# Kernel optimization log

Hardware: AMD Instinct MI355X
Metric: run time of the kernel (lower is better)

Reference implementation:

```python
import jax, jax.numpy as jnp
import numpy as np

HIDDEN = 1024
H = 16        # query heads
HK = 4        # kv heads
G = H // HK   # GQA group size
D = 64        # head dim
EPS = 1e-6


def rmsnorm(x, w):
    # normalize over last dim (head_dim)
    var = jnp.mean(jnp.square(x), axis=-1, keepdims=True)
    return x * jax.lax.rsqrt(var + EPS) * w


def setup_inputs() -> dict:
    key = jax.random.key(0)
    ks = jax.random.split(key, 8)
    B, S_KV, S_Q = 2, 4096, 512
    inputs = jax.random.normal(ks[0], (B, S_KV, HIDDEN), dtype=jnp.float32)
    latent = jax.random.normal(ks[1], (B, S_Q, HIDDEN), dtype=jnp.float32)
    # xavier_uniform-style init: limit = sqrt(6/(fan_in+fan_out))
    def xavier(k, shape, gain=1.0):
        fan_out, fan_in = shape
        limit = gain * np.sqrt(6.0 / (fan_in + fan_out))
        return jax.random.uniform(k, shape, jnp.float32, -limit, limit)
    wq = xavier(ks[2], (H * D, HIDDEN))
    wk = xavier(ks[3], (HK * D, HIDDEN))
    wv = xavier(ks[4], (HK * D, HIDDEN))
    wo = xavier(ks[5], (HIDDEN, H * D), gain=1.0 / np.sqrt(2.0))
    q_norm_w = jnp.ones((D,), jnp.float32)
    k_norm_w = jnp.ones((D,), jnp.float32)
    return {"inputs": inputs, "latent": latent, "wq": wq, "wk": wk,
            "wv": wv, "wo": wo, "q_norm_w": q_norm_w, "k_norm_w": k_norm_w}


def reference(inputs, latent, wq, wk, wv, wo, q_norm_w, k_norm_w):
    B, S_q, _ = latent.shape
    S_kv = inputs.shape[1]
    # projections (Linear: x @ W^T)
    q = (latent @ wq.T).reshape(B, S_q, H, D)    # [B,Sq,H,D]
    k = (inputs @ wk.T).reshape(B, S_kv, HK, D)  # [B,Skv,Hk,D]
    v = (inputs @ wv.T).reshape(B, S_kv, HK, D)
    q = rmsnorm(q, q_norm_w)
    k = rmsnorm(k, k_norm_w)
    # GQA without materializing repeated K/V: view q as [B,Hk,G,Sq,D]
    q = q.transpose(0, 2, 1, 3).reshape(B, HK, G, S_q, D)
    k = k.transpose(0, 2, 1, 3)  # [B,Hk,Skv,D]
    v = v.transpose(0, 2, 1, 3)  # [B,Hk,Skv,D]
    # NOTE: no 1/sqrt(D) scaling, faithful to the source module
    scores = jnp.einsum('bkgqd,bksd->bkgqs', q, k)  # [B,Hk,G,Sq,Skv]
    attn = jax.nn.softmax(scores.astype(jnp.float32), axis=-1).astype(q.dtype)
    out = jnp.einsum('bkgqs,bksd->bkgqd', attn, v)  # [B,Hk,G,Sq,D]
    # back to [B,Sq,H*D]
    out = out.reshape(B, H, S_q, D).transpose(0, 2, 1, 3).reshape(B, S_q, H * D)
    return out @ wo.T
```

## Files before the change

kernel.cpp:

```cpp
#include <hip/hip_runtime.h>

#define NB 2
#define SQ 512
#define SKV 4096
#define HID 1024
#define NH 16
#define NHK 4
#define NG 4
#define HD 64
#define EPSF 1e-6f
#define NSPLIT 4
#define RB (NB * NH * SQ)

typedef short v8s __attribute__((ext_vector_type(8)));
typedef short v4s __attribute__((ext_vector_type(4)));
typedef float v4f __attribute__((ext_vector_type(4)));
typedef float v2f __attribute__((ext_vector_type(2)));

static __device__ __forceinline__ short f2bf(float f) {
  unsigned u = __builtin_bit_cast(unsigned, f);
  u += 0x7FFFu + ((u >> 16) & 1u);
  return (short)(u >> 16);
}

static __device__ __forceinline__ v8s lds_frag(const short* lds, int row, int kbyte) {
  return *(const v8s*)((const char*)lds + row * 128 + (kbyte ^ ((row & 7) << 4)));
}

template<int SRC_F32, int NIT>
static __device__ __forceinline__ void stage_tile(const void* src, int ld,
                                                  int r0, int c0, short* lds, int t) {
#pragma unroll
  for (int i = 0; i < NIT; ++i) {
    int flat = t * 8 + i * 2048;
    int row = flat >> 6, col = flat & 63;
    v8s v;
    if (SRC_F32) {
      const float* p = (const float*)src + (size_t)(r0 + row) * ld + c0 + col;
      v4f a = *(const v4f*)p;
      v4f b = *(const v4f*)(p + 4);
      v[0] = f2bf(a[0]); v[1] = f2bf(a[1]); v[2] = f2bf(a[2]); v[3] = f2bf(a[3]);
      v[4] = f2bf(b[0]); v[5] = f2bf(b[1]); v[6] = f2bf(b[2]); v[7] = f2bf(b[3]);
    } else {
      v = *(const v8s*)((const short*)src + (size_t)(r0 + row) * ld + c0 + col);
    }
    *(v8s*)((char*)lds + row * 128 + ((col * 2) ^ ((row & 7) << 4))) = v;
  }
}

__global__ __launch_bounds__(256) void proj_all(const float* __restrict__ inputs,
                                                const float* __restrict__ latent,
                                                const float* __restrict__ wq,
                                                const float* __restrict__ wk,
                                                const float* __restrict__ wv,
                                                const float* __restrict__ qnw,
                                                const float* __restrict__ knw,
                                                short* __restrict__ Qb,
                                                short* __restrict__ Kb,
                                                short* __restrict__ Vtb) {
  __shared__ __align__(16) short Asm[128 * 64];
  __shared__ __align__(16) short Bsm[128 * 64];
  const int bid = blockIdx.x;
  const int t = threadIdx.x, lane = t & 63, w = t >> 6;
  const int l15 = lane & 15, g4 = lane >> 4;
  v4f acc[2][4] = {};

  if (bid < 512) {
    const int xcd = bid & 7, slot = bid >> 3;
    const int mblk = xcd * 8 + (slot >> 3);
    const int zh = slot & 7;
    const int z = zh & 1, head = zh >> 1;
    const int m0 = mblk * 128;
    const float* W = z ? wv : wk;
    for (int k0 = 0; k0 < HID; k0 += 64) {
      __syncthreads();
      stage_tile<1, 4>(inputs, HID, m0, k0, Asm, t);
      stage_tile<1, 2>(W, HID, head * 64, k0, Bsm, t);
      __syncthreads();
      v8s af[2][2], bfr[4][2];
#pragma unroll
      for (int mf = 0; mf < 2; ++mf)
#pragma unroll
        for (int s = 0; s < 2; ++s)
          af[mf][s] = lds_frag(Asm, w * 32 + mf * 16 + l15, s * 64 + g4 * 16);
#pragma unroll
      for (int nf = 0; nf < 4; ++nf)
#pragma unroll
        for (int s = 0; s < 2; ++s)
          bfr[nf][s] = lds_frag(Bsm, nf * 16 + l15, s * 64 + g4 * 16);
#pragma unroll
      for (int mf = 0; mf < 2; ++mf)
#pragma unroll
        for (int nf = 0; nf < 4; ++nf)
#pragma unroll
          for (int s = 0; s < 2; ++s)
            acc[mf][nf] = __builtin_amdgcn_mfma_f32_16x16x32_bf16(af[mf][s], bfr[nf][s],
                                                                  acc[mf][nf], 0, 0, 0);
    }
    if (!z) {
      float wcol[4];
#pragma unroll
      for (int nf = 0; nf < 4; ++nf) wcol[nf] = knw[nf * 16 + l15];
#pragma unroll
      for (int mf = 0; mf < 2; ++mf)
#pragma unroll
        for (int j = 0; j < 4; ++j) {
          float ss = acc[mf][0][j] * acc[mf][0][j] + acc[mf][1][j] * acc[mf][1][j] +
                     acc[mf][2][j] * acc[mf][2][j] + acc[mf][3][j] * acc[mf][3][j];
#pragma unroll
          for (int msk = 1; msk < 16; msk <<= 1) ss += __shfl_xor(ss, msk);
          float sc = rsqrtf(ss * (1.0f / 64.0f) + EPSF);
          int m = m0 + w * 32 + mf * 16 + g4 * 4 + j;
          int b = m >> 12, sl = m & (SKV - 1);
          size_t base = ((size_t)(b * NHK + head) * SKV + sl) * 64;
#pragma unroll
          for (int nf = 0; nf < 4; ++nf)
            Kb[base + nf * 16 + l15] = f2bf(acc[mf][nf][j] * sc * wcol[nf]);
        }
    } else {
#pragma unroll
      for (int mf = 0; mf < 2; ++mf) {
        int m = m0 + w * 32 + mf * 16 + g4 * 4;
        int b = m >> 12, sl = m & (SKV - 1);
#pragma unroll
        for (int nf = 0; nf < 4; ++nf) {
          int d = nf * 16 + l15;
          v4s o;
#pragma unroll
          for (int j = 0; j < 4; ++j) o[j] = f2bf(acc[mf][nf][j]);
          *(v4s*)(Vtb + ((size_t)(b * NHK + head) * 64 + d) * SKV + sl) = o;
        }
      }
    }
  } else {
    const int r = bid - 512;
    const int xcd = r & 7, slot = r >> 3;
    const int nblk = (slot & 1) | ((xcd & 3) << 1);
    const int mblk = ((slot >> 1) & 7) | ((xcd >> 2) << 3);
    const int m0 = mblk * 64;
    const int wr = w >> 1, wc = w & 1;
    for (int k0 = 0; k0 < HID; k0 += 64) {
      __syncthreads();
      stage_tile<1, 2>(latent, HID, m0, k0, Asm, t);
      stage_tile<1, 4>(wq, HID, nblk * 128, k0, Bsm, t);
      __syncthreads();
      v8s af[2][2], bfr[4][2];
#pragma unroll
      for (int mf = 0; mf < 2; ++mf)
#pragma unroll
        for (int s = 0; s < 2; ++s)
          af[mf][s] = lds_frag(Asm, wr * 32 + mf * 16 + l15, s * 64 + g4 * 16);
#pragma unroll
      for (int nf = 0; nf < 4; ++nf)
#pragma unroll
        for (int s = 0; s < 2; ++s)
          bfr[nf][s] = lds_frag(Bsm, wc * 64 + nf * 16 + l15, s * 64 + g4 * 16);
#pragma unroll
      for (int mf = 0; mf < 2; ++mf)
#pragma unroll
        for (int nf = 0; nf < 4; ++nf)
#pragma unroll
          for (int s = 0; s < 2; ++s)
            acc[mf][nf] = __builtin_amdgcn_mfma_f32_16x16x32_bf16(af[mf][s], bfr[nf][s],
                                                                  acc[mf][nf], 0, 0, 0);
    }
    const int head = nblk * 2 + wc;
    float wcol[4];
#pragma unroll
    for (int nf = 0; nf < 4; ++nf) wcol[nf] = qnw[nf * 16 + l15];
#pragma unroll
    for (int mf = 0; mf < 2; ++mf)
#pragma unroll
      for (int j = 0; j < 4; ++j) {
        float ss = acc[mf][0][j] * acc[mf][0][j] + acc[mf][1][j] * acc[mf][1][j] +
                   acc[mf][2][j] * acc[mf][2][j] + acc[mf][3][j] * acc[mf][3][j];
#pragma unroll
        for (int msk = 1; msk < 16; msk <<= 1) ss += __shfl_xor(ss, msk);
        float sc = rsqrtf(ss * (1.0f / 64.0f) + EPSF);
        int m = m0 + wr * 32 + mf * 16 + g4 * 4 + j;
        int b = m >> 9, sl = m & (SQ - 1);
        size_t base = ((size_t)(b * NH + head) * SQ + sl) * 64;
#pragma unroll
        for (int nf = 0; nf < 4; ++nf)
          Qb[base + nf * 16 + l15] = f2bf(acc[mf][nf][j] * sc * wcol[nf]);
      }
  }
}

__global__ __launch_bounds__(256) void wo_gemm(const short* __restrict__ Ab,
                                               const float* __restrict__ Wo,
                                               float* __restrict__ Wop) {
  __shared__ __align__(16) short Asm[64 * 64];
  __shared__ __align__(16) short Bsm[128 * 64];
  const int t = threadIdx.x, lane = t & 63, w = t >> 6;
  const int l15 = lane & 15, g4 = lane >> 4;
  const int wr = w >> 1, wc = w & 1;
  const int p = blockIdx.x;
  const int nblk = p & 7, slot = p >> 3;
  const int m0 = (slot & 15) * 64, n0 = nblk * 128, ks = slot >> 4;
  v4f acc[2][4] = {};
  for (int kk = 0; kk < 4; ++kk) {
    int k0 = ks * 256 + kk * 64;
    __syncthreads();
    stage_tile<0, 2>(Ab, HID, m0, k0, Asm, t);
    stage_tile<1, 4>(Wo, HID, n0, k0, Bsm, t);
    __syncthreads();
    v8s af[2][2], bfr[4][2];
#pragma unroll
    for (int mf = 0; mf < 2; ++mf)
#pragma unroll
      for (int s = 0; s < 2; ++s)
        af[mf][s] = lds_frag(Asm, wr * 32 + mf * 16 + l15, s * 64 + g4 * 16);
#pragma unroll
    for (int nf = 0; nf < 4; ++nf)
#pragma unroll
      for (int s = 0; s < 2; ++s)
        bfr[nf][s] = lds_frag(Bsm, wc * 64 + nf * 16 + l15, s * 64 + g4 * 16);
#pragma unroll
    for (int mf = 0; mf < 2; ++mf)
#pragma unroll
      for (int nf = 0; nf < 4; ++nf)
#pragma unroll
        for (int s = 0; s < 2; ++s)
          acc[mf][nf] = __builtin_amdgcn_mfma_f32_16x16x32_bf16(af[mf][s], bfr[nf][s],
                                                                acc[mf][nf], 0, 0, 0);
  }
  float* C = Wop + (size_t)ks * HID * NB * SQ;
#pragma unroll
  for (int mf = 0; mf < 2; ++mf)
#pragma unroll
    for (int j = 0; j < 4; ++j) {
      int m = m0 + wr * 32 + mf * 16 + g4 * 4 + j;
#pragma unroll
      for (int nf = 0; nf < 4; ++nf)
        C[(size_t)m * HID + n0 + wc * 64 + nf * 16 + l15] = acc[mf][nf][j];
    }
}

__global__ __launch_bounds__(256) void wo_reduce(const float* __restrict__ Wop,
                                                 float* __restrict__ out) {
  int idx = (blockIdx.x * 256 + threadIdx.x) * 4;
  v4f s = *(const v4f*)(Wop + idx);
#pragma unroll
  for (int ks = 1; ks < 4; ++ks) {
    v4f p = *(const v4f*)(Wop + (size_t)ks * HID * NB * SQ + idx);
    s[0] += p[0]; s[1] += p[1]; s[2] += p[2]; s[3] += p[3];
  }
  *(v4f*)(out + idx) = s;
}

__global__ __launch_bounds__(256) void attn_kernel(const short* __restrict__ Qb,
                                                   const short* __restrict__ Kb,
                                                   const short* __restrict__ Vt,
                                                   float* __restrict__ Op,
                                                   float* __restrict__ Ml) {
  __shared__ __align__(16) short Ksm[2][64 * 64];
  __shared__ __align__(16) short Vsm[2][64 * 64];
  __shared__ __align__(16) short Psm[4][16 * 64];
  int id = blockIdx.x;
  int qt = id & 31, hk = (id >> 5) & 3, b = (id >> 7) & 1, sp = id >> 8;
  int t = threadIdx.x, w = t >> 6, lane = t & 63;
  int l15 = lane & 15, g4 = lane >> 4;
  int h = hk * NG + w;

  const short* qbase = Qb + (((size_t)(b * NH + h)) * SQ + qt * 16) * 64;
  v8s aq[2];
#pragma unroll
  for (int s = 0; s < 2; ++s)
    aq[s] = *(const v8s*)(qbase + (size_t)l15 * 64 + s * 32 + g4 * 8);

  const short* kbase = Kb + ((size_t)(b * NHK + hk)) * SKV * 64;
  const short* vbase = Vt + ((size_t)(b * NHK + hk)) * 64 * SKV;
  char* pbase = (char*)&Psm[w][0];

  v4f acco[4] = {};
  float mrow[4], lrow[4];
#pragma unroll
  for (int r = 0; r < 4; ++r) { mrow[r] = -__builtin_inff(); lrow[r] = 0.f; }

  const int KV0 = sp * (SKV / NSPLIT);
  for (int kt = 0; kt < SKV / NSPLIT / 128; ++kt) {
    int kv0 = KV0 + kt * 128;
    __syncthreads();
    stage_tile<0, 2>(kbase, 64, kv0, 0, Ksm[0], t);
    stage_tile<0, 2>(kbase, 64, kv0 + 64, 0, Ksm[1], t);
    stage_tile<0, 2>(vbase, SKV, 0, kv0, Vsm[0], t);
    stage_tile<0, 2>(vbase, SKV, 0, kv0 + 64, Vsm[1], t);
    __syncthreads();

    v4f accs[8] = {};
#pragma unroll
    for (int hf = 0; hf < 2; ++hf)
#pragma unroll
      for (int f = 0; f < 4; ++f)
#pragma unroll
        for (int s = 0; s < 2; ++s) {
          v8s bk = lds_frag(Ksm[hf], f * 16 + l15, s * 64 + g4 * 16);
          accs[hf * 4 + f] =
              __builtin_amdgcn_mfma_f32_16x16x32_bf16(aq[s], bk, accs[hf * 4 + f], 0, 0, 0);
        }

    float tm[4];
#pragma unroll
    for (int r = 0; r < 4; ++r) {
      float m01 = fmaxf(accs[0][r], accs[1][r]), m23 = fmaxf(accs[2][r], accs[3][r]);
      float m45 = fmaxf(accs[4][r], accs[5][r]), m67 = fmaxf(accs[6][r], accs[7][r]);
      tm[r] = fmaxf(fmaxf(m01, m23), fmaxf(m45, m67));
    }
#pragma unroll
    for (int msk = 1; msk < 16; msk <<= 1)
#pragma unroll
      for (int r = 0; r < 4; ++r)
        tm[r] = fmaxf(tm[r], __shfl_xor(tm[r], msk));
    float al[4];
#pragma unroll
    for (int r = 0; r < 4; ++r) {
      float mn = fmaxf(mrow[r], tm[r]);
      al[r] = __expf(mrow[r] - mn);
      mrow[r] = mn;
    }
    float rs[4] = {0.f, 0.f, 0.f, 0.f};
#pragma unroll
    for (int f = 0; f < 8; ++f)
#pragma unroll
      for (int r = 0; r < 4; ++r) {
        accs[f][r] = __expf(accs[f][r] - mrow[r]);
        rs[r] += accs[f][r];
      }
#pragma unroll
    for (int msk = 1; msk < 16; msk <<= 1)
#pragma unroll
      for (int r = 0; r < 4; ++r) rs[r] += __shfl_xor(rs[r], msk);
#pragma unroll
    for (int r = 0; r < 4; ++r) lrow[r] = lrow[r] * al[r] + rs[r];
#pragma unroll
    for (int fd = 0; fd < 4; ++fd)
#pragma unroll
      for (int r = 0; r < 4; ++r) acco[fd][r] *= al[r];

#pragma unroll
    for (int hf = 0; hf < 2; ++hf) {
#pragma unroll
      for (int f = 0; f < 4; ++f)
#pragma unroll
        for (int r = 0; r < 4; ++r) {
          int row = g4 * 4 + r;
          int colB = (f * 16 + l15) * 2;
          *(short*)(pbase + row * 128 + (colB ^ ((row & 7) << 4))) = f2bf(accs[hf * 4 + f][r]);
        }
      asm volatile("s_waitcnt lgkmcnt(0)" ::: "memory");
      __builtin_amdgcn_sched_barrier(0);
      v8s pa[2];
#pragma unroll
      for (int s = 0; s < 2; ++s)
        pa[s] = *(const v8s*)(pbase + l15 * 128 + ((s * 64 + g4 * 16) ^ ((l15 & 7) << 4)));
      asm volatile("s_waitcnt lgkmcnt(0)" ::: "memory");
      __builtin_amdgcn_sched_barrier(0);
#pragma unroll
      for (int fd = 0; fd < 4; ++fd)
#pragma unroll
        for (int s = 0; s < 2; ++s) {
          v8s vb = lds_frag(Vsm[hf], fd * 16 + l15, s * 64 + g4 * 16);
          acco[fd] = __builtin_amdgcn_mfma_f32_16x16x32_bf16(pa[s], vb, acco[fd], 0, 0, 0);
        }
    }
  }

  size_t rowbase = ((size_t)b * NH + h) * SQ + qt * 16;
#pragma unroll
  for (int fd = 0; fd < 4; ++fd)
#pragma unroll
    for (int r = 0; r < 4; ++r) {
      int row = g4 * 4 + r;
      Op[((size_t)sp * RB + rowbase + row) * 64 + fd * 16 + l15] = acco[fd][r];
    }
  if (l15 == 0) {
#pragma unroll
    for (int r = 0; r < 4; ++r) {
      int row = g4 * 4 + r;
      v2f ml; ml[0] = mrow[r]; ml[1] = lrow[r];
      *(v2f*)(Ml + ((size_t)sp * RB + rowbase + row) * 2) = ml;
    }
  }
}

__global__ __launch_bounds__(256) void merge_attn(const float* __restrict__ Op,
                                                  const float* __restrict__ Ml,
                                                  short* __restrict__ Ab) {
  int idx = blockIdx.x * 256 + threadIdx.x;
  int d = idx & 63, row = idx >> 6;
  float ms[NSPLIT], ls[NSPLIT];
  float M = -__builtin_inff();
#pragma unroll
  for (int s = 0; s < NSPLIT; ++s) {
    v2f ml = *(const v2f*)(Ml + ((size_t)s * RB + row) * 2);
    ms[s] = ml[0]; ls[s] = ml[1];
    M = fmaxf(M, ms[s]);
  }
  float L = 0.f, o = 0.f;
#pragma unroll
  for (int s = 0; s < NSPLIT; ++s) {
    float wgt = __expf(ms[s] - M);
    L += ls[s] * wgt;
    o += wgt * Op[((size_t)s * RB + row) * 64 + d];
  }
  int b = row >> 13;
  int hh = (row >> 9) & 15;
  int sq = row & 511;
  Ab[((size_t)(b * SQ + sq)) * HID + hh * 64 + d] = f2bf(o / L);
}

extern "C" void kernel_launch(void* const* d_in, const int* in_sizes, int n_in,
                              void* d_out, int out_size, void* d_ws, size_t ws_size,
                              hipStream_t stream) {
  const float* inputs = (const float*)d_in[0];
  const float* latent = (const float*)d_in[1];
  const float* wq = (const float*)d_in[2];
  const float* wk = (const float*)d_in[3];
  const float* wv = (const float*)d_in[4];
  const float* wo = (const float*)d_in[5];
  const float* qnw = (const float*)d_in[6];
  const float* knw = (const float*)d_in[7];

  char* ws = (char*)d_ws;
  float* Op  = (float*)(ws);
  float* Wop = (float*)(ws);
  float* Ml  = (float*)(ws + 16777216);
  short* Qb  = (short*)(ws + 17825792);
  short* Kb  = (short*)(ws + 19922944);
  short* Vtb = (short*)(ws + 24117248);
  short* Ab  = (short*)(ws + 28311552);

  proj_all<<<640, 256, 0, stream>>>(inputs, latent, wq, wk, wv, qnw, knw, Qb, Kb, Vtb);
  attn_kernel<<<256 * NSPLIT, 256, 0, stream>>>(Qb, Kb, Vtb, Op, Ml);
  merge_attn<<<RB * 64 / 256, 256, 0, stream>>>(Op, Ml, Ab);
  wo_gemm<<<512, 256, 0, stream>>>(Ab, wo, Wop);
  wo_reduce<<<1024, 256, 0, stream>>>(Wop, (float*)d_out);
}
```

Before: 213.9 us.

## Double-buffer LDS with register prefetch in projection and output GEMMs

Adds software pipelining to the projection and Wo GEMM kernels. Global loads for the next K tile are issued into registers before the current tile's MFMAs run, and are converted and written into the other LDS buffer afterwards. This drops one barrier per iteration and hides global-load latency behind compute. In exchange, LDS use rises to two 24KB buffers and register pressure grows from the prefetch registers, which may lower occupancy. The attention kernel only gets a renamed staging helper.

```diff
diff --git a/kernel.cpp b/kernel.cpp
--- a/kernel.cpp
+++ b/kernel.cpp
@@ -27,26 +27,68 @@
   return *(const v8s*)((const char*)lds + row * 128 + (kbyte ^ ((row & 7) << 4)));
 }
 
-template<int SRC_F32, int NIT>
-static __device__ __forceinline__ void stage_tile(const void* src, int ld,
-                                                  int r0, int c0, short* lds, int t) {
+template<int NIT>
+static __device__ __forceinline__ void stage_load_f32(const float* src, int ld,
+                                                      int r0, int c0, int t, v4f* regs) {
 #pragma unroll
   for (int i = 0; i < NIT; ++i) {
     int flat = t * 8 + i * 2048;
     int row = flat >> 6, col = flat & 63;
+    const float* p = src + (size_t)(r0 + row) * ld + c0 + col;
+    regs[2 * i] = *(const v4f*)p;
+    regs[2 * i + 1] = *(const v4f*)(p + 4);
+  }
+}
+
+template<int NIT>
+static __device__ __forceinline__ void stage_write_bf16(const v4f* regs, short* lds, int t) {
+#pragma unroll
+  for (int i = 0; i < NIT; ++i) {
+    int flat = t * 8 + i * 2048;
+    int row = flat >> 6, col = flat & 63;
+    v4f a = regs[2 * i], b = regs[2 * i + 1];
     v8s v;
-    if (SRC_F32) {
-      const float* p = (const float*)src + (size_t)(r0 + row) * ld + c0 + col;
-      v4f a = *(const v4f*)p;
-      v4f b = *(const v4f*)(p + 4);
-      v[0] = f2bf(a[0]); v[1] = f2bf(a[1]); v[2] = f2bf(a[2]); v[3] = f2bf(a[3]);
-      v[4] = f2bf(b[0]); v[5] = f2bf(b[1]); v[6] = f2bf(b[2]); v[7] = f2bf(b[3]);
-    } else {
-      v = *(const v8s*)((const short*)src + (size_t)(r0 + row) * ld + c0 + col);
-    }
+    v[0] = f2bf(a[0]); v[1] = f2bf(a[1]); v[2] = f2bf(a[2]); v[3] = f2bf(a[3]);
+    v[4] = f2bf(b[0]); v[5] = f2bf(b[1]); v[6] = f2bf(b[2]); v[7] = f2bf(b[3]);
     *(v8s*)((char*)lds + row * 128 + ((col * 2) ^ ((row & 7) << 4))) = v;
   }
 }
+
+template<int NIT>
+static __device__ __forceinline__ void stage_load_bf16(const short* src, int ld,
+                                                       int r0, int c0, int t, v8s* regs) {
+#pragma unroll
+  for (int i = 0; i < NIT; ++i) {
+    int flat = t * 8 + i * 2048;
+    int row = flat >> 6, col = flat & 63;
+    regs[i] = *(const v8s*)(src + (size_t)(r0 + row) * ld + c0 + col);
+  }
+}
+
+template<int NIT>
+static __device__ __forceinline__ void stage_write_raw(const v8s* regs, short* lds, int t) {
+#pragma unroll
+  for (int i = 0; i < NIT; ++i) {
+    int flat = t * 8 + i * 2048;
+    int row = flat >> 6, col = flat & 63;
+    *(v8s*)((char*)lds + row * 128 + ((col * 2) ^ ((row & 7) << 4))) = regs[i];
+  }
+}
+
+template<int NIT>
+static __device__ __forceinline__ void stage_tile_b(const short* src, int ld,
+                                                    int r0, int c0, short* lds, int t) {
+#pragma unroll
+  for (int i = 0; i < NIT; ++i) {
+    int flat = t * 8 + i * 2048;
+    int row = flat >> 6, col = flat & 63;
+    v8s v = *(const v8s*)(src + (size_t)(r0 + row) * ld + c0 + col);
+    *(v8s*)((char*)lds + row * 128 + ((col * 2) ^ ((row & 7) << 4))) = v;
+  }
+}
+
+#define KV_ASZ (128 * 64)
+#define Q_ASZ (64 * 64)
 
 __global__ __launch_bounds__(256) void proj_all(const float* __restrict__ inputs,
                                                 const float* __restrict__ latent,
@@ -58,8 +100,7 @@
                                                 short* __restrict__ Qb,
                                                 short* __restrict__ Kb,
                                                 short* __restrict__ Vtb) {
-  __shared__ __align__(16) short Asm[128 * 64];
-  __shared__ __align__(16) short Bsm[128 * 64];
+  __shared__ __align__(16) short smem[2][192 * 64];
   const int bid = blockIdx.x;
   const int t = threadIdx.x, lane = t & 63, w = t >> 6;
   const int l15 = lane & 15, g4 = lane >> 4;
@@ -72,22 +113,29 @@
     const int z = zh & 1, head = zh >> 1;
     const int m0 = mblk * 128;
     const float* W = z ? wv : wk;
-    for (int k0 = 0; k0 < HID; k0 += 64) {
+    v4f ar[8], br[4];
+    stage_load_f32<4>(inputs, HID, m0, 0, t, ar);
+    stage_load_f32<2>(W, HID, head * 64, 0, t, br);
+    stage_write_bf16<4>(ar, &smem[0][0], t);
+    stage_write_bf16<2>(br, &smem[0][KV_ASZ], t);
+    for (int kt = 0; kt < 16; ++kt) {
       __syncthreads();
-      stage_tile<1, 4>(inputs, HID, m0, k0, Asm, t);
-      stage_tile<1, 2>(W, HID, head * 64, k0, Bsm, t);
-      __syncthreads();
+      const short* Acur = &smem[kt & 1][0];
+      const short* Bcur = &smem[kt & 1][KV_ASZ];
+      int kn = ((kt + 1) & 15) * 64;
+      stage_load_f32<4>(inputs, HID, m0, kn, t, ar);
+      stage_load_f32<2>(W, HID, head * 64, kn, t, br);
       v8s af[2][2], bfr[4][2];
 #pragma unroll
       for (int mf = 0; mf < 2; ++mf)
 #pragma unroll
         for (int s = 0; s < 2; ++s)
-          af[mf][s] = lds_frag(Asm, w * 32 + mf * 16 + l15, s * 64 + g4 * 16);
+          af[mf][s] = lds_frag(Acur, w * 32 + mf * 16 + l15, s * 64 + g4 * 16);
 #pragma unroll
       for (int nf = 0; nf < 4; ++nf)
 #pragma unroll
         for (int s = 0; s < 2; ++s)
-          bfr[nf][s] = lds_frag(Bsm, nf * 16 + l15, s * 64 + g4 * 16);
+          bfr[nf][s] = lds_frag(Bcur, nf * 16 + l15, s * 64 + g4 * 16);
 #pragma unroll
       for (int mf = 0; mf < 2; ++mf)
 #pragma unroll
@@ -96,6 +144,11 @@
           for (int s = 0; s < 2; ++s)
             acc[mf][nf] = __builtin_amdgcn_mfma_f32_16x16x32_bf16(af[mf][s], bfr[nf][s],
                                                                   acc[mf][nf], 0, 0, 0);
+      if (kt + 1 < 16) {
+        short* An = &smem[(kt + 1) & 1][0];
+        stage_write_bf16<4>(ar, An, t);
+        stage_write_bf16<2>(br, An + KV_ASZ, t);
+      }
     }
     if (!z) {
       float wcol[4];
@@ -139,22 +192,29 @@
     const int mblk = ((slot >> 1) & 7) | ((xcd >> 2) << 3);
     const int m0 = mblk * 64;
     const int wr = w >> 1, wc = w & 1;
-    for (int k0 = 0; k0 < HID; k0 += 64) {
+    v4f ar[4], br[8];
+    stage_load_f32<2>(latent, HID, m0, 0, t, ar);
+    stage_load_f32<4>(wq, HID, nblk * 128, 0, t, br);
+    stage_write_bf16<2>(ar, &smem[0][0], t);
+    stage_write_bf16<4>(br, &smem[0][Q_ASZ], t);
+    for (int kt = 0; kt < 16; ++kt) {
       __syncthreads();
-      stage_tile<1, 2>(latent, HID, m0, k0, Asm, t);
-      stage_tile<1, 4>(wq, HID, nblk * 128, k0, Bsm, t);
-      __syncthreads();
+      const short* Acur = &smem[kt & 1][0];
+      const short* Bcur = &smem[kt & 1][Q_ASZ];
+      int kn = ((kt + 1) & 15) * 64;
+      stage_load_f32<2>(latent, HID, m0, kn, t, ar);
+      stage_load_f32<4>(wq, HID, nblk * 128, kn, t, br);
       v8s af[2][2], bfr[4][2];
 #pragma unroll
       for (int mf = 0; mf < 2; ++mf)
 #pragma unroll
         for (int s = 0; s < 2; ++s)
-          af[mf][s] = lds_frag(Asm, wr * 32 + mf * 16 + l15, s * 64 + g4 * 16);
+          af[mf][s] = lds_frag(Acur, wr * 32 + mf * 16 + l15, s * 64 + g4 * 16);
 #pragma unroll
       for (int nf = 0; nf < 4; ++nf)
 #pragma unroll
         for (int s = 0; s < 2; ++s)
-          bfr[nf][s] = lds_frag(Bsm, wc * 64 + nf * 16 + l15, s * 64 + g4 * 16);
+          bfr[nf][s] = lds_frag(Bcur, wc * 64 + nf * 16 + l15, s * 64 + g4 * 16);
 #pragma unroll
       for (int mf = 0; mf < 2; ++mf)
 #pragma unroll
@@ -163,6 +223,11 @@
           for (int s = 0; s < 2; ++s)
             acc[mf][nf] = __builtin_amdgcn_mfma_f32_16x16x32_bf16(af[mf][s], bfr[nf][s],
                                                                   acc[mf][nf], 0, 0, 0);
+      if (kt + 1 < 16) {
+        short* An = &smem[(kt + 1) & 1][0];
+        stage_write_bf16<2>(ar, An, t);
+        stage_write_bf16<4>(br, An + Q_ASZ, t);
+      }
     }
     const int head = nblk * 2 + wc;
     float wcol[4];
@@ -190,8 +255,7 @@
 __global__ __launch_bounds__(256) void wo_gemm(const short* __restrict__ Ab,
                                                const float* __restrict__ Wo,
                                                float* __restrict__ Wop) {
-  __shared__ __align__(16) short Asm[64 * 64];
-  __shared__ __align__(16) short Bsm[128 * 64];
+  __shared__ __align__(16) short smem[2][192 * 64];
   const int t = threadIdx.x, lane = t & 63, w = t >> 6;
   const int l15 = lane & 15, g4 = lane >> 4;
   const int wr = w >> 1, wc = w & 1;
@@ -199,23 +263,30 @@
   const int nblk = p & 7, slot = p >> 3;
   const int m0 = (slot & 15) * 64, n0 = nblk * 128, ks = slot >> 4;
   v4f acc[2][4] = {};
+  v8s ar[2];
+  v4f br[8];
+  stage_load_bf16<2>(Ab, HID, m0, ks * 256, t, ar);
+  stage_load_f32<4>(Wo, HID, n0, ks * 256, t, br);
+  stage_write_raw<2>(ar, &smem[0][0], t);
+  stage_write_bf16<4>(br, &smem[0][Q_ASZ], t);
   for (int kk = 0; kk < 4; ++kk) {
-    int k0 = ks * 256 + kk * 64;
     __syncthreads();
-    stage_tile<0, 2>(Ab, HID, m0, k0, Asm, t);
-    stage_tile<1, 4>(Wo, HID, n0, k0, Bsm, t);
-    __syncthreads();
+    const short* Acur = &smem[kk & 1][0];
+    const short* Bcur = &smem[kk & 1][Q_ASZ];
+    int kn = ks * 256 + ((kk + 1) & 3) * 64;
+    stage_load_bf16<2>(Ab, HID, m0, kn, t, ar);
+    stage_load_f32<4>(Wo, HID, n0, kn, t, br);
     v8s af[2][2], bfr[4][2];
 #pragma unroll
     for (int mf = 0; mf < 2; ++mf)
 #pragma unroll
       for (int s = 0; s < 2; ++s)
-        af[mf][s] = lds_frag(Asm, wr * 32 + mf * 16 + l15, s * 64 + g4 * 16);
+        af[mf][s] = lds_frag(Acur, wr * 32 + mf * 16 + l15, s * 64 + g4 * 16);
 #pragma unroll
     for (int nf = 0; nf < 4; ++nf)
 #pragma unroll
       for (int s = 0; s < 2; ++s)
-        bfr[nf][s] = lds_frag(Bsm, wc * 64 + nf * 16 + l15, s * 64 + g4 * 16);
+        bfr[nf][s] = lds_frag(Bcur, wc * 64 + nf * 16 + l15, s * 64 + g4 * 16);
 #pragma unroll
     for (int mf = 0; mf < 2; ++mf)
 #pragma unroll
@@ -224,6 +295,11 @@
         for (int s = 0; s < 2; ++s)
           acc[mf][nf] = __builtin_amdgcn_mfma_f32_16x16x32_bf16(af[mf][s], bfr[nf][s],
                                                                 acc[mf][nf], 0, 0, 0);
+    if (kk + 1 < 4) {
+      short* An = &smem[(kk + 1) & 1][0];
+      stage_write_raw<2>(ar, An, t);
+      stage_write_bf16<4>(br, An + Q_ASZ, t);
+    }
   }
   float* C = Wop + (size_t)ks * HID * NB * SQ;
 #pragma unroll
@@ -282,10 +358,10 @@
   for (int kt = 0; kt < SKV / NSPLIT / 128; ++kt) {
     int kv0 = KV0 + kt * 128;
     __syncthreads();
-    stage_tile<0, 2>(kbase, 64, kv0, 0, Ksm[0], t);
-    stage_tile<0, 2>(kbase, 64, kv0 + 64, 0, Ksm[1], t);
-    stage_tile<0, 2>(vbase, SKV, 0, kv0, Vsm[0], t);
-    stage_tile<0, 2>(vbase, SKV, 0, kv0 + 64, Vsm[1], t);
+    stage_tile_b<2>(kbase, 64, kv0, 0, Ksm[0], t);
+    stage_tile_b<2>(kbase, 64, kv0 + 64, 0, Ksm[1], t);
+    stage_tile_b<2>(vbase, SKV, 0, kv0, Vsm[0], t);
+    stage_tile_b<2>(vbase, SKV, 0, kv0 + 64, Vsm[1], t);
     __syncthreads();
 
     v4f accs[8] = {};
```

Measured after the change: 199.8 us. 1.07x faster.
